# Kernel tuning notes

Hardware: AMD Instinct MI355X
Metric: run time of the kernel (lower is better)

## Reference

```python
import jax, jax.numpy as jnp
import numpy as np

B, C, H, W = 4, 256, 64, 64
CQK = C // 8  # qk_downscale = 8


def setup_inputs() -> dict:
    key = jax.random.key(0)
    ks = jax.random.split(key, 4)
    scale = 0.02
    x = jax.random.normal(ks[0], (B, C, H, W), dtype=jnp.float32)
    Wq = jax.random.normal(ks[1], (CQK, C), dtype=jnp.float32) * scale
    bq = jnp.zeros((CQK,), dtype=jnp.float32)
    Wk = jax.random.normal(ks[2], (CQK, C), dtype=jnp.float32) * scale
    bk = jnp.zeros((CQK,), dtype=jnp.float32)
    Wv = jax.random.normal(ks[3], (C, C), dtype=jnp.float32) * scale
    bv = jnp.zeros((C,), dtype=jnp.float32)
    gamma = jnp.ones((1,), dtype=jnp.float32)
    return {"x": x, "Wq": Wq, "bq": bq, "Wk": Wk, "bk": bk,
            "Wv": Wv, "bv": bv, "gamma": gamma}


def reference(x, Wq, bq, Wk, bk, Wv, bv, gamma):
    b, c, h, w = x.shape
    n = h * w
    xf = x.reshape(b, c, n)                                   # [B,C,N]
    # 1x1 Conv1d == per-position linear projection
    q = jnp.einsum('oc,bcn->bon', Wq, xf) + bq[:, None]        # [B,C/8,N]
    k = jnp.einsum('oc,bcn->bon', Wk, xf) + bk[:, None]        # [B,C/8,N]
    v = jnp.einsum('oc,bcn->bon', Wv, xf) + bv[:, None]        # [B,C,N]
    # scores[b,i,j] = sum_c q[b,c,i] * k[b,c,j]  (bmm(q^T, k))
    scores = jnp.einsum('bci,bcj->bij', q, k)                  # [B,N,N]
    # softmax over dim=1 (the i / contracted axis) — SAGAN style, no 1/sqrt(d)
    attn = jax.nn.softmax(scores, axis=1)                      # [B,N,N]
    out = gamma * jnp.einsum('bcn,bnm->bcm', v, attn) + xf     # [B,C,N]
    return out.reshape(b, c, h, w)
```

## Files before the change

### kernel.cpp

```cpp
#include <hip/hip_runtime.h>
#include <stdint.h>

typedef __attribute__((ext_vector_type(8))) short short8;
typedef __attribute__((ext_vector_type(4))) float f32x4;
typedef __attribute__((ext_vector_type(4))) unsigned int u32x4;

#define MFMA16(a, b, c) __builtin_amdgcn_mfma_f32_16x16x32_bf16((a), (b), (c), 0, 0, 0)

#define GLOAD_LDS16(gsrc, ldst)                                                        \
    __builtin_amdgcn_global_load_lds(                                                  \
        (const __attribute__((address_space(1))) unsigned int*)(gsrc),                 \
        (__attribute__((address_space(3))) unsigned int*)(ldst), 16, 0, 0)

#define LOG2E 1.4426950408889634f

static __device__ __forceinline__ unsigned short f2bf(float f) {
    union { float f; unsigned int u; } v; v.f = f;
    unsigned int u = v.u;
    unsigned int r = 0x7fffu + ((u >> 16) & 1u);
    return (unsigned short)((u + r) >> 16);
}

static __device__ __forceinline__ float bf2f(unsigned short s) {
    union { unsigned int u; float f; } v; v.u = ((unsigned int)s) << 16;
    return v.f;
}

static __device__ __forceinline__ unsigned int cvt_pk_bf16(float lo, float hi) {
    unsigned int r;
    asm("v_cvt_pk_bf16_f32 %0, %1, %2" : "=v"(r) : "v"(lo), "v"(hi));
    return r;
}

static __device__ __forceinline__ float fexp2(float x) {
#if __has_builtin(__builtin_amdgcn_exp2f)
    return __builtin_amdgcn_exp2f(x);
#else
    return exp2f(x);
#endif
}

__global__ __launch_bounds__(256) void k_prepw(const float* __restrict__ Wq,
                                               const float* __restrict__ Wk,
                                               const float* __restrict__ Wv,
                                               unsigned short* __restrict__ Wb) {
    const int i = (blockIdx.x * 256 + threadIdx.x) * 4;
    const float* src; int off;
    if (i < 8192)       { src = Wq; off = i; }
    else if (i < 16384) { src = Wk; off = i - 8192; }
    else                { src = Wv; off = i - 16384; }
    const float4 v = *(const float4*)(src + off);
    ushort4 o;
    o.x = f2bf(v.x); o.y = f2bf(v.y); o.z = f2bf(v.z); o.w = f2bf(v.w);
    *(ushort4*)(Wb + i) = o;
}

__global__ __launch_bounds__(256) void k_qkv(const float* __restrict__ x,
                                             const unsigned short* __restrict__ Wb,
                                             const float* __restrict__ bq,
                                             const float* __restrict__ bk,
                                             const float* __restrict__ bv,
                                             unsigned short* __restrict__ qT,
                                             unsigned short* __restrict__ kT,
                                             unsigned short* __restrict__ vp) {
    const int b = blockIdx.y;
    const int nt = blockIdx.x;
    const int h = blockIdx.z;
    const int lane = threadIdx.x & 63;
    const int wv = threadIdx.x >> 6;
    const int l15 = lane & 15, g = lane >> 4;
    const int n0 = nt * 64;
    const int nw = n0 + wv * 16;

    const float* xb = x + (size_t)b * 1048576;
    const float* xs = xb + (size_t)(g * 8) * 4096 + nw + l15;

    const unsigned short* Wqb = Wb;
    const unsigned short* Wkb = Wb + 8192;
    const unsigned short* Wvb = Wb + 16384 + h * 32768;

    f32x4 aqk[4] = {};
    f32x4 av[8] = {};

#pragma unroll 2
    for (int k0 = 0; k0 < 256; k0 += 32) {
        const float* xp = xs + (size_t)k0 * 4096;
        float xv[8];
#pragma unroll
        for (int j = 0; j < 8; ++j) xv[j] = xp[(size_t)j * 4096];
        const u32x4 ux = {cvt_pk_bf16(xv[0], xv[1]), cvt_pk_bf16(xv[2], xv[3]),
                          cvt_pk_bf16(xv[4], xv[5]), cvt_pk_bf16(xv[6], xv[7])};
        const short8 xa = __builtin_bit_cast(short8, ux);

        if (h == 0) {
#pragma unroll
            for (int ot = 0; ot < 4; ++ot) {
                const unsigned short* wr = (ot < 2) ? (Wqb + (size_t)(ot * 16 + l15) * 256)
                                                    : (Wkb + (size_t)((ot - 2) * 16 + l15) * 256);
                const short8 wb8 = *(const short8*)(wr + k0 + g * 8);
                aqk[ot] = MFMA16(xa, wb8, aqk[ot]);
            }
        }
#pragma unroll
        for (int ct = 0; ct < 8; ++ct) {
            const short8 wv8 = *(const short8*)(Wvb + (size_t)(ct * 16 + l15) * 256 + k0 + g * 8);
            av[ct] = MFMA16(wv8, xa, av[ct]);
        }
    }

    if (h == 0) {
#pragma unroll
        for (int ot = 0; ot < 4; ++ot) {
            const int o = (ot & 1) * 16 + l15;
            const float bias = (ot < 2) ? bq[o] : bk[o];
            const float sc = (ot < 2) ? LOG2E : 1.0f;
            unsigned short* dst = (ot < 2) ? qT : kT;
#pragma unroll
            for (int r = 0; r < 4; ++r) {
                const int n = nw + g * 4 + r;
                dst[((size_t)b * 4096 + n) * 32 + o] = f2bf((aqk[ot][r] + bias) * sc);
            }
        }
    }
    const int jp = ((wv >> 1) * 4 + (l15 >> 2)) * 8 + (wv & 1) * 4 + (l15 & 3);
#pragma unroll
    for (int ct = 0; ct < 8; ++ct)
#pragma unroll
        for (int r = 0; r < 4; ++r) {
            const int c = h * 128 + ct * 16 + g * 4 + r;
            vp[((size_t)b * 256 + c) * 4096 + n0 + jp] = f2bf(av[ct][r] + bv[c]);
        }
}

__global__ __launch_bounds__(256, 2) void k_attn(const unsigned short* __restrict__ qT,
                                                 const unsigned short* __restrict__ kT,
                                                 const unsigned short* __restrict__ vp,
                                                 unsigned short* __restrict__ Opart,
                                                 float* __restrict__ mll,
                                                 int ilen) {
    __shared__ __align__(16) unsigned short vlds[2 * 16384];

    const int b = blockIdx.y;
    const int mt = blockIdx.x;
    const int sp = blockIdx.z;
    const int tid = threadIdx.x;
    const int lane = tid & 63;
    const int wv = tid >> 6;
    const int l15 = lane & 15, g = lane >> 4;
    const int m_base = mt * 128 + wv * 32;
    const int i_start = sp * ilen;
    const int T = ilen >> 6;

    const unsigned short* qTb = qT + (size_t)b * 131072;
    const unsigned short* vpb = vp + (size_t)b * 1048576;

    const short8 qkB0 = *(const short8*)(kT + ((size_t)b * 4096 + m_base + l15) * 32 + g * 8);
    const short8 qkB1 = *(const short8*)(kT + ((size_t)b * 4096 + m_base + 16 + l15) * 32 + g * 8);

    const int jd = (lane & 7) ^ ((lane >> 3) & 7);
    const unsigned short* vsrc = vpb + (size_t)(64 * wv + (lane >> 3)) * 4096 + i_start + jd * 8;
    const int ldst0 = wv * 4096;

#define STAGE(bufsel, ioff)                                                             \
    do {                                                                                \
        _Pragma("unroll")                                                               \
        for (int s_ = 0; s_ < 8; ++s_)                                                  \
            GLOAD_LDS16(vsrc + (size_t)s_ * 32768 + (ioff),                             \
                        vlds + (bufsel) * 16384 + ldst0 + s_ * 512);                    \
    } while (0)

    const int rdA = l15 * 64 + ((g ^ (l15 & 7)) << 3);
    const int rdB = l15 * 64 + (((4 + g) ^ (l15 & 7)) << 3);

    const unsigned short* qp = qTb + (size_t)(i_start + l15) * 32 + g * 8;

    f32x4 oacc[16][2] = {};
    float l_acc0 = 0.0f, l_acc1 = 0.0f;
    const f32x4 zf = {0.f, 0.f, 0.f, 0.f};

    STAGE(0, 0);
    short8 qa0 = *(const short8*)(qp);
    short8 qa1 = *(const short8*)(qp + 512);
    short8 qa2 = *(const short8*)(qp + 1024);
    short8 qa3 = *(const short8*)(qp + 1536);
    qp += 2048;
    __syncthreads();

    for (int t = 0; t < T; ++t) {
        const int cur = t & 1;
        if (t + 1 < T) STAGE(cur ^ 1, (t + 1) * 64);

        f32x4 P[4][2];
        P[0][0] = MFMA16(qa0, qkB0, zf); P[0][1] = MFMA16(qa0, qkB1, zf);
        P[1][0] = MFMA16(qa1, qkB0, zf); P[1][1] = MFMA16(qa1, qkB1, zf);
        P[2][0] = MFMA16(qa2, qkB0, zf); P[2][1] = MFMA16(qa2, qkB1, zf);
        P[3][0] = MFMA16(qa3, qkB0, zf); P[3][1] = MFMA16(qa3, qkB1, zf);

        float s00 = 0.f, s01 = 0.f, s10 = 0.f, s11 = 0.f;
#pragma unroll
        for (int it = 0; it < 4; ++it)
#pragma unroll
            for (int r = 0; r < 4; ++r) {
                P[it][0][r] = fexp2(P[it][0][r]);
                P[it][1][r] = fexp2(P[it][1][r]);
                if (it < 2) { s00 += P[it][0][r]; s01 += P[it][1][r]; }
                else        { s10 += P[it][0][r]; s11 += P[it][1][r]; }
            }
        l_acc0 += s00 + s10;
        l_acc1 += s01 + s11;

        const u32x4 u00 = {cvt_pk_bf16(P[0][0][0], P[0][0][1]), cvt_pk_bf16(P[0][0][2], P[0][0][3]),
                           cvt_pk_bf16(P[1][0][0], P[1][0][1]), cvt_pk_bf16(P[1][0][2], P[1][0][3])};
        const u32x4 u01 = {cvt_pk_bf16(P[0][1][0], P[0][1][1]), cvt_pk_bf16(P[0][1][2], P[0][1][3]),
                           cvt_pk_bf16(P[1][1][0], P[1][1][1]), cvt_pk_bf16(P[1][1][2], P[1][1][3])};
        const u32x4 u10 = {cvt_pk_bf16(P[2][0][0], P[2][0][1]), cvt_pk_bf16(P[2][0][2], P[2][0][3]),
                           cvt_pk_bf16(P[3][0][0], P[3][0][1]), cvt_pk_bf16(P[3][0][2], P[3][0][3])};
        const u32x4 u11 = {cvt_pk_bf16(P[2][1][0], P[2][1][1]), cvt_pk_bf16(P[2][1][2], P[2][1][3]),
                           cvt_pk_bf16(P[3][1][0], P[3][1][1]), cvt_pk_bf16(P[3][1][2], P[3][1][3])};
        const short8 pb00 = __builtin_bit_cast(short8, u00);
        const short8 pb01 = __builtin_bit_cast(short8, u01);
        const short8 pb10 = __builtin_bit_cast(short8, u10);
        const short8 pb11 = __builtin_bit_cast(short8, u11);

        short8 qn0, qn1, qn2, qn3;
        if (t + 1 < T) {
            qn0 = *(const short8*)(qp);
            qn1 = *(const short8*)(qp + 512);
            qn2 = *(const short8*)(qp + 1024);
            qn3 = *(const short8*)(qp + 1536);
            qp += 2048;
        }

        const unsigned short* vbase = vlds + cur * 16384;
        const unsigned short* pA = vbase + rdA;
        const unsigned short* pB = vbase + rdB;
        __builtin_amdgcn_s_setprio(1);
#pragma unroll
        for (int ct = 0; ct < 16; ++ct) {
            const short8 va0 = *(const short8*)(pA + ct * 1024);
            const short8 va1 = *(const short8*)(pB + ct * 1024);
            oacc[ct][0] = MFMA16(va0, pb00, oacc[ct][0]);
            oacc[ct][1] = MFMA16(va0, pb01, oacc[ct][1]);
            oacc[ct][0] = MFMA16(va1, pb10, oacc[ct][0]);
            oacc[ct][1] = MFMA16(va1, pb11, oacc[ct][1]);
        }
        __builtin_amdgcn_s_setprio(0);

        if (t + 1 < T) {
            qa0 = qn0; qa1 = qn1; qa2 = qn2; qa3 = qn3;
            __syncthreads();
        }
    }
#undef STAGE

    unsigned short* Ob = Opart + (size_t)(sp * 4 + b) * 1048576;
#pragma unroll
    for (int ct = 0; ct < 16; ++ct)
#pragma unroll
        for (int r = 0; r < 4; ++r) {
            const int c = ct * 16 + g * 4 + r;
            Ob[(size_t)c * 4096 + m_base + l15]      = f2bf(oacc[ct][0][r]);
            Ob[(size_t)c * 4096 + m_base + 16 + l15] = f2bf(oacc[ct][1][r]);
        }
    float l0 = l_acc0, l1 = l_acc1;
    l0 += __shfl_xor(l0, 16); l0 += __shfl_xor(l0, 32);
    l1 += __shfl_xor(l1, 16); l1 += __shfl_xor(l1, 32);
    if (lane < 16) {
        const size_t mi = (size_t)(sp * 4 + b) * 4096 + m_base + l15;
        mll[mi]      = l0;
        mll[mi + 16] = l1;
    }
}

__global__ __launch_bounds__(256) void k_combine(const unsigned short* __restrict__ Opart,
                                                 const float* __restrict__ mll,
                                                 const float* __restrict__ x,
                                                 const float* __restrict__ gamma,
                                                 float* __restrict__ out, int S) {
    const size_t e0 = ((size_t)blockIdx.x * 256 + threadIdx.x) * 8;
    const int m0 = (int)(e0 & 4095);
    const int b = (int)(e0 >> 20);

    float L[8] = {}, O[8] = {};
    for (int s = 0; s < S; ++s) {
        const size_t base = (size_t)(s * 4 + b) * 4096 + m0;
        const float4 la = *(const float4*)(mll + base);
        const float4 lc = *(const float4*)(mll + base + 4);
        const short8 op = *(const short8*)(Opart + (size_t)s * 4194304 + e0);
        L[0] += la.x; O[0] += bf2f((unsigned short)op[0]);
        L[1] += la.y; O[1] += bf2f((unsigned short)op[1]);
        L[2] += la.z; O[2] += bf2f((unsigned short)op[2]);
        L[3] += la.w; O[3] += bf2f((unsigned short)op[3]);
        L[4] += lc.x; O[4] += bf2f((unsigned short)op[4]);
        L[5] += lc.y; O[5] += bf2f((unsigned short)op[5]);
        L[6] += lc.z; O[6] += bf2f((unsigned short)op[6]);
        L[7] += lc.w; O[7] += bf2f((unsigned short)op[7]);
    }

    const float g0 = gamma[0];
    const float4 x0 = *(const float4*)(x + e0);
    const float4 x1 = *(const float4*)(x + e0 + 4);
    float4 o0, o1;
    o0.x = g0 * O[0] / L[0] + x0.x; o0.y = g0 * O[1] / L[1] + x0.y;
    o0.z = g0 * O[2] / L[2] + x0.z; o0.w = g0 * O[3] / L[3] + x0.w;
    o1.x = g0 * O[4] / L[4] + x1.x; o1.y = g0 * O[5] / L[5] + x1.y;
    o1.z = g0 * O[6] / L[6] + x1.z; o1.w = g0 * O[7] / L[7] + x1.w;
    *(float4*)(out + e0) = o0;
    *(float4*)(out + e0 + 4) = o1;
}

extern "C" void kernel_launch(void* const* d_in, const int* in_sizes, int n_in,
                              void* d_out, int out_size, void* d_ws, size_t ws_size,
                              hipStream_t stream) {
    (void)in_sizes; (void)n_in; (void)out_size;
    const float* x     = (const float*)d_in[0];
    const float* Wq    = (const float*)d_in[1];
    const float* bq    = (const float*)d_in[2];
    const float* Wk    = (const float*)d_in[3];
    const float* bk    = (const float*)d_in[4];
    const float* Wv    = (const float*)d_in[5];
    const float* bv    = (const float*)d_in[6];
    const float* gamma = (const float*)d_in[7];
    float* out = (float*)d_out;

    unsigned short* qT = (unsigned short*)d_ws;
    unsigned short* kT = qT + (size_t)4 * 4096 * 32;
    unsigned short* vp = kT + (size_t)4 * 4096 * 32;
    unsigned short* Wb = vp + (size_t)4 * 256 * 4096;
    unsigned short* Opart = Wb + 81920;

    const size_t base_el = 2 * (size_t)4 * 4096 * 32 + (size_t)4 * 256 * 4096 + 81920;
    auto need = [&](int s) {
        return (base_el + (size_t)s * 4194304) * 2 + (size_t)s * 16384 * 4;
    };
    const int S = (need(4) <= ws_size) ? 4 : (need(2) <= ws_size) ? 2 : 1;
    float* mll = (float*)(Opart + (size_t)S * 4194304);

    k_prepw<<<dim3(80), 256, 0, stream>>>(Wq, Wk, Wv, Wb);
    k_qkv<<<dim3(64, 4, 2), 256, 0, stream>>>(x, Wb, bq, bk, bv, qT, kT, vp);
    k_attn<<<dim3(32, 4, S), 256, 0, stream>>>(qT, kT, vp, Opart, mll, 4096 / S);
    k_combine<<<dim3(2048), 256, 0, stream>>>(Opart, mll, x, gamma, out, S);
}
```

Before: 83.74 us.

## Store V and attention probabilities in FP8 and use FP8 MFMA for PV

```diff
diff --git a/kernel.cpp b/kernel.cpp
--- a/kernel.cpp
+++ b/kernel.cpp
@@ -4,8 +4,10 @@
 typedef __attribute__((ext_vector_type(8))) short short8;
 typedef __attribute__((ext_vector_type(4))) float f32x4;
 typedef __attribute__((ext_vector_type(4))) unsigned int u32x4;
+typedef __attribute__((ext_vector_type(2))) unsigned int u32x2;
 
 #define MFMA16(a, b, c) __builtin_amdgcn_mfma_f32_16x16x32_bf16((a), (b), (c), 0, 0, 0)
+#define MFMAF8(a, b, c) __builtin_amdgcn_mfma_f32_16x16x32_fp8_fp8((a), (b), (c), 0, 0, 0)
 
 #define GLOAD_LDS16(gsrc, ldst)                                                        \
     __builtin_amdgcn_global_load_lds(                                                  \
@@ -37,6 +39,43 @@
     return __builtin_amdgcn_exp2f(x);
 #else
     return exp2f(x);
+#endif
+}
+
+static __device__ __forceinline__ unsigned char f2e4m3_sw(float x) {
+    unsigned u = __builtin_bit_cast(unsigned, x);
+    unsigned s = (u >> 24) & 0x80u;
+    float ax = fabsf(x);
+    if (ax > 448.f) return (unsigned char)(s | 0x7e);
+    if (ax < 0.0078125f) {
+        int m = (int)(ax * 512.f + 0.5f);
+        return (unsigned char)(s | m);
+    }
+    int e = (int)((u >> 23) & 0xff) - 127;
+    unsigned m = (u >> 20) & 7;
+    m += (u >> 19) & 1;
+    unsigned enc = (unsigned)((e + 7) << 3) + m;
+    if (enc > 0x7e) enc = 0x7e;
+    return (unsigned char)(s | enc);
+}
+
+static __device__ __forceinline__ unsigned int pk_fp8_4(float a, float b, float c, float d) {
+#if __has_builtin(__builtin_amdgcn_cvt_pk_fp8_f32)
+    int r = 0;
+    r = __builtin_amdgcn_cvt_pk_fp8_f32(a, b, r, false);
+    r = __builtin_amdgcn_cvt_pk_fp8_f32(c, d, r, true);
+    return (unsigned int)r;
+#else
+    return (unsigned)f2e4m3_sw(a) | ((unsigned)f2e4m3_sw(b) << 8) |
+           ((unsigned)f2e4m3_sw(c) << 16) | ((unsigned)f2e4m3_sw(d) << 24);
+#endif
+}
+
+static __device__ __forceinline__ unsigned char f2fp8(float v) {
+#if __has_builtin(__builtin_amdgcn_cvt_pk_fp8_f32)
+    return (unsigned char)(__builtin_amdgcn_cvt_pk_fp8_f32(v, v, 0, false) & 0xff);
+#else
+    return f2e4m3_sw(v);
 #endif
 }
 
@@ -62,7 +101,7 @@
                                              const float* __restrict__ bv,
                                              unsigned short* __restrict__ qT,
                                              unsigned short* __restrict__ kT,
-                                             unsigned short* __restrict__ vp) {
+                                             unsigned char* __restrict__ vp8) {
     const int b = blockIdx.y;
     const int nt = blockIdx.x;
     const int h = blockIdx.z;
@@ -128,17 +167,17 @@
 #pragma unroll
         for (int r = 0; r < 4; ++r) {
             const int c = h * 128 + ct * 16 + g * 4 + r;
-            vp[((size_t)b * 256 + c) * 4096 + n0 + jp] = f2bf(av[ct][r] + bv[c]);
+            vp8[((size_t)b * 256 + c) * 4096 + n0 + jp] = f2fp8(av[ct][r] + bv[c]);
         }
 }
 
 __global__ __launch_bounds__(256, 2) void k_attn(const unsigned short* __restrict__ qT,
                                                  const unsigned short* __restrict__ kT,
-                                                 const unsigned short* __restrict__ vp,
+                                                 const unsigned char* __restrict__ vp8,
                                                  unsigned short* __restrict__ Opart,
                                                  float* __restrict__ mll,
                                                  int ilen) {
-    __shared__ __align__(16) unsigned short vlds[2 * 16384];
+    __shared__ __align__(16) unsigned char vlds[2 * 16384];
 
     const int b = blockIdx.y;
     const int mt = blockIdx.x;
@@ -152,25 +191,25 @@
     const int T = ilen >> 6;
 
     const unsigned short* qTb = qT + (size_t)b * 131072;
-    const unsigned short* vpb = vp + (size_t)b * 1048576;
+    const unsigned char* vpb8 = vp8 + (size_t)b * 1048576;
 
     const short8 qkB0 = *(const short8*)(kT + ((size_t)b * 4096 + m_base + l15) * 32 + g * 8);
     const short8 qkB1 = *(const short8*)(kT + ((size_t)b * 4096 + m_base + 16 + l15) * 32 + g * 8);
 
-    const int jd = (lane & 7) ^ ((lane >> 3) & 7);
-    const unsigned short* vsrc = vpb + (size_t)(64 * wv + (lane >> 3)) * 4096 + i_start + jd * 8;
+    const unsigned char* vsrc = vpb8 + (size_t)(64 * wv + (lane >> 2)) * 4096 + i_start
+                              + (size_t)(((2 * (lane & 3)) ^ ((lane >> 2) & 6)) * 8);
     const int ldst0 = wv * 4096;
 
 #define STAGE(bufsel, ioff)                                                             \
     do {                                                                                \
         _Pragma("unroll")                                                               \
-        for (int s_ = 0; s_ < 8; ++s_)                                                  \
-            GLOAD_LDS16(vsrc + (size_t)s_ * 32768 + (ioff),                             \
-                        vlds + (bufsel) * 16384 + ldst0 + s_ * 512);                    \
+        for (int s_ = 0; s_ < 4; ++s_)                                                  \
+            GLOAD_LDS16(vsrc + (size_t)s_ * 65536 + (ioff),                             \
+                        vlds + (bufsel) * 16384 + ldst0 + s_ * 1024);                   \
     } while (0)
 
-    const int rdA = l15 * 64 + ((g ^ (l15 & 7)) << 3);
-    const int rdB = l15 * 64 + (((4 + g) ^ (l15 & 7)) << 3);
+    const int rdA = l15 * 64 + ((g ^ (l15 & 6)) << 3);
+    const int rdB = l15 * 64 + (((4 + g) ^ (l15 & 6)) << 3);
 
     const unsigned short* qp = qTb + (size_t)(i_start + l15) * 32 + g * 8;
 
@@ -209,18 +248,18 @@
         l_acc0 += s00 + s10;
         l_acc1 += s01 + s11;
 
-        const u32x4 u00 = {cvt_pk_bf16(P[0][0][0], P[0][0][1]), cvt_pk_bf16(P[0][0][2], P[0][0][3]),
-                           cvt_pk_bf16(P[1][0][0], P[1][0][1]), cvt_pk_bf16(P[1][0][2], P[1][0][3])};
-        const u32x4 u01 = {cvt_pk_bf16(P[0][1][0], P[0][1][1]), cvt_pk_bf16(P[0][1][2], P[0][1][3]),
-                           cvt_pk_bf16(P[1][1][0], P[1][1][1]), cvt_pk_bf16(P[1][1][2], P[1][1][3])};
-        const u32x4 u10 = {cvt_pk_bf16(P[2][0][0], P[2][0][1]), cvt_pk_bf16(P[2][0][2], P[2][0][3]),
-                           cvt_pk_bf16(P[3][0][0], P[3][0][1]), cvt_pk_bf16(P[3][0][2], P[3][0][3])};
-        const u32x4 u11 = {cvt_pk_bf16(P[2][1][0], P[2][1][1]), cvt_pk_bf16(P[2][1][2], P[2][1][3]),
-                           cvt_pk_bf16(P[3][1][0], P[3][1][1]), cvt_pk_bf16(P[3][1][2], P[3][1][3])};
-        const short8 pb00 = __builtin_bit_cast(short8, u00);
-        const short8 pb01 = __builtin_bit_cast(short8, u01);
-        const short8 pb10 = __builtin_bit_cast(short8, u10);
-        const short8 pb11 = __builtin_bit_cast(short8, u11);
+        const u32x2 w00 = {pk_fp8_4(P[0][0][0], P[0][0][1], P[0][0][2], P[0][0][3]),
+                           pk_fp8_4(P[1][0][0], P[1][0][1], P[1][0][2], P[1][0][3])};
+        const u32x2 w01 = {pk_fp8_4(P[0][1][0], P[0][1][1], P[0][1][2], P[0][1][3]),
+                           pk_fp8_4(P[1][1][0], P[1][1][1], P[1][1][2], P[1][1][3])};
+        const u32x2 w10 = {pk_fp8_4(P[2][0][0], P[2][0][1], P[2][0][2], P[2][0][3]),
+                           pk_fp8_4(P[3][0][0], P[3][0][1], P[3][0][2], P[3][0][3])};
+        const u32x2 w11 = {pk_fp8_4(P[2][1][0], P[2][1][1], P[2][1][2], P[2][1][3]),
+                           pk_fp8_4(P[3][1][0], P[3][1][1], P[3][1][2], P[3][1][3])};
+        const long pf00 = __builtin_bit_cast(long, w00);
+        const long pf01 = __builtin_bit_cast(long, w01);
+        const long pf10 = __builtin_bit_cast(long, w10);
+        const long pf11 = __builtin_bit_cast(long, w11);
 
         short8 qn0, qn1, qn2, qn3;
         if (t + 1 < T) {
@@ -231,18 +270,18 @@
             qp += 2048;
         }
 
-        const unsigned short* vbase = vlds + cur * 16384;
-        const unsigned short* pA = vbase + rdA;
-        const unsigned short* pB = vbase + rdB;
+        const unsigned char* vbase = vlds + cur * 16384;
+        const unsigned char* pA = vbase + rdA;
+        const unsigned char* pB = vbase + rdB;
         __builtin_amdgcn_s_setprio(1);
 #pragma unroll
         for (int ct = 0; ct < 16; ++ct) {
-            const short8 va0 = *(const short8*)(pA + ct * 1024);
-            const short8 va1 = *(const short8*)(pB + ct * 1024);
-            oacc[ct][0] = MFMA16(va0, pb00, oacc[ct][0]);
-            oacc[ct][1] = MFMA16(va0, pb01, oacc[ct][1]);
-            oacc[ct][0] = MFMA16(va1, pb10, oacc[ct][0]);
-            oacc[ct][1] = MFMA16(va1, pb11, oacc[ct][1]);
+            const long va0 = __builtin_bit_cast(long, *(const u32x2*)(pA + ct * 1024));
+            const long va1 = __builtin_bit_cast(long, *(const u32x2*)(pB + ct * 1024));
+            oacc[ct][0] = MFMAF8(va0, pf00, oacc[ct][0]);
+            oacc[ct][1] = MFMAF8(va0, pf01, oacc[ct][1]);
+            oacc[ct][0] = MFMAF8(va1, pf10, oacc[ct][0]);
+            oacc[ct][1] = MFMAF8(va1, pf11, oacc[ct][1]);
         }
         __builtin_amdgcn_s_setprio(0);
 
@@ -325,11 +364,11 @@
 
     unsigned short* qT = (unsigned short*)d_ws;
     unsigned short* kT = qT + (size_t)4 * 4096 * 32;
-    unsigned short* vp = kT + (size_t)4 * 4096 * 32;
-    unsigned short* Wb = vp + (size_t)4 * 256 * 4096;
+    unsigned char* vp8 = (unsigned char*)(kT + (size_t)4 * 4096 * 32);
+    unsigned short* Wb = (unsigned short*)(vp8 + (size_t)4 * 256 * 4096);
     unsigned short* Opart = Wb + 81920;
 
-    const size_t base_el = 2 * (size_t)4 * 4096 * 32 + (size_t)4 * 256 * 4096 + 81920;
+    const size_t base_el = 2 * (size_t)4 * 4096 * 32 + 2097152 + 81920;
     auto need = [&](int s) {
         return (base_el + (size_t)s * 4194304) * 2 + (size_t)s * 16384 * 4;
     };
@@ -337,7 +376,7 @@
     float* mll = (float*)(Opart + (size_t)S * 4194304);
 
     k_prepw<<<dim3(80), 256, 0, stream>>>(Wq, Wk, Wv, Wb);
-    k_qkv<<<dim3(64, 4, 2), 256, 0, stream>>>(x, Wb, bq, bk, bv, qT, kT, vp);
-    k_attn<<<dim3(32, 4, S), 256, 0, stream>>>(qT, kT, vp, Opart, mll, 4096 / S);
+    k_qkv<<<dim3(64, 4, 2), 256, 0, stream>>>(x, Wb, bq, bk, bv, qT, kT, vp8);
+    k_attn<<<dim3(32, 4, S), 256, 0, stream>>>(qT, kT, vp8, Opart, mll, 4096 / S);
     k_combine<<<dim3(2048), 256, 0, stream>>>(Opart, mll, x, gamma, out, S);
 }
```

After: 78.87 us. -5.8%, faster.
